# Optimization experiments

Measured on AMD Instinct MI355X. Metric: run time of the kernel, lower is better.

Reference implementation:

```python
import jax, jax.numpy as jnp
import numpy as np

EMB = 1024
HEADS = 16
HEADSIZE = EMB // HEADS
LN_EPS = 1e-5


def layernorm(x, w, b):
    # normalize over last dim (headsize)
    mu = jnp.mean(x, axis=-1, keepdims=True)
    var = jnp.var(x, axis=-1, keepdims=True)
    return (x - mu) * jax.lax.rsqrt(var + LN_EPS) * w + b


def setup_inputs() -> dict:
    key = jax.random.key(0)
    ks = jax.random.split(key, 8)
    B, S, C = 2, 2048, 2048
    x = jax.random.normal(ks[0], (B, S, EMB), dtype=jnp.float32)
    context = jax.random.normal(ks[1], (B, C, EMB), dtype=jnp.float32)
    mask = jnp.ones((B, S), dtype=jnp.float32)
    contextMask = jnp.ones((B, C), dtype=jnp.float32)
    s = 0.02
    Wq = jax.random.normal(ks[2], (EMB, EMB), dtype=jnp.float32) * s
    Wk = jax.random.normal(ks[3], (EMB, EMB), dtype=jnp.float32) * s
    Wv = jax.random.normal(ks[4], (EMB, EMB), dtype=jnp.float32) * s
    Wu = jax.random.normal(ks[5], (EMB, EMB), dtype=jnp.float32) * s
    bu = jnp.zeros((EMB,), dtype=jnp.float32)
    qln_w = jnp.ones((HEADSIZE,), dtype=jnp.float32)
    qln_b = jnp.zeros((HEADSIZE,), dtype=jnp.float32)
    kln_w = jnp.ones((HEADSIZE,), dtype=jnp.float32)
    kln_b = jnp.zeros((HEADSIZE,), dtype=jnp.float32)
    return {"x": x, "context": context, "mask": mask, "contextMask": contextMask,
            "Wq": Wq, "Wk": Wk, "Wv": Wv, "Wu": Wu, "bu": bu,
            "qln_w": qln_w, "qln_b": qln_b, "kln_w": kln_w, "kln_b": kln_b}


def reference(x, context, mask, contextMask, Wq, Wk, Wv, Wu, bu, qln_w, qln_b, kln_w, kln_b):
    B, S, E = x.shape
    C = context.shape[1]
    T = S + C
    xc = jnp.concatenate([x, context], axis=1)            # [B, T, E]
    q = (x @ Wq).reshape(B, S, HEADS, HEADSIZE)
    k = (xc @ Wk).reshape(B, T, HEADS, HEADSIZE)
    v = (xc @ Wv).reshape(B, T, HEADS, HEADSIZE)
    q = layernorm(q, qln_w, qln_b)
    k = layernorm(k, kln_w, kln_b)
    scale = E ** 0.25
    q = q / scale
    k = k / scale
    # [B, H, S, T] score matrix (explicitly materialized, as in the original)
    dot = jnp.einsum('bshd,bthd->bhst', q, k)
    mcat = jnp.concatenate([mask, contextMask], axis=1)   # [B, T]
    dotMask = mask[:, None, :, None] * mcat[:, None, None, :]  # [B,1,S,T]
    # hand-rolled masked softmax: softmax(dot*mask) * mask, renormalize
    p = jax.nn.softmax(dot * dotMask, axis=-1) * dotMask
    p = p / (jnp.sum(p, axis=-1, keepdims=True) + 1e-13)
    out = jnp.einsum('bhst,bthd->bshd', p, v).reshape(B, S, E)
    return out @ Wu + bu
```

## Files before the change

### kernel.cpp

```cpp
#include <hip/hip_runtime.h>
#include <hip/hip_bf16.h>
#include <cstdint>

#define B_SZ   2
#define S_LEN  2048
#define C_LEN  2048
#define T_LEN  4096
#define EMB_   1024
#define HEADS_ 16
#define D_     64

typedef __attribute__((ext_vector_type(8))) short bf16x8;
typedef __attribute__((ext_vector_type(4))) float f32x4;
typedef __attribute__((ext_vector_type(16))) float f32x16;
typedef __attribute__((ext_vector_type(2))) float f32x2;

__device__ __forceinline__ unsigned short f2bf(float f) {
    unsigned u = __builtin_bit_cast(unsigned, f);
    u += 0x7fffu + ((u >> 16) & 1u);
    return (unsigned short)(u >> 16);
}
__device__ __forceinline__ float bf2f(unsigned short h) {
    return __builtin_bit_cast(float, (unsigned)h << 16);
}

__global__ void build_xcb_k(const float* __restrict__ x, const float* __restrict__ ctx,
                            unsigned short* __restrict__ xcb) {
    int i = blockIdx.x * blockDim.x + threadIdx.x;
    size_t e8 = (size_t)i * 8;
    int b = (int)(e8 / ((size_t)T_LEN * EMB_));
    size_t rem = e8 % ((size_t)T_LEN * EMB_);
    int t = (int)(rem / EMB_);
    int c = (int)(rem % EMB_);
    const float* src = (t < S_LEN)
        ? &x[((size_t)b * S_LEN + t) * EMB_ + c]
        : &ctx[((size_t)b * C_LEN + (t - S_LEN)) * EMB_ + c];
    float4 v0 = ((const float4*)src)[0];
    float4 v1 = ((const float4*)src)[1];
    uint4 o;
    o.x = (unsigned)f2bf(v0.x) | ((unsigned)f2bf(v0.y) << 16);
    o.y = (unsigned)f2bf(v0.z) | ((unsigned)f2bf(v0.w) << 16);
    o.z = (unsigned)f2bf(v1.x) | ((unsigned)f2bf(v1.y) << 16);
    o.w = (unsigned)f2bf(v1.z) | ((unsigned)f2bf(v1.w) << 16);
    *(uint4*)&xcb[e8] = o;
}

__global__ void mcat_k(const float* __restrict__ mask, const float* __restrict__ cmask,
                       float* __restrict__ Mcat) {
    int i = blockIdx.x * 256 + threadIdx.x;
    int b = i / T_LEN, t = i % T_LEN;
    Mcat[i] = (t < S_LEN) ? mask[(size_t)b * S_LEN + t]
                          : cmask[(size_t)b * C_LEN + (t - S_LEN)];
}

__global__ void wtrans4_k(const float* __restrict__ W0, const float* __restrict__ W1,
                          const float* __restrict__ W2, const float* __restrict__ W3,
                          unsigned short* __restrict__ T0, unsigned short* __restrict__ T1,
                          unsigned short* __restrict__ T2, unsigned short* __restrict__ T3) {
    __shared__ __align__(16) unsigned short tile[64][72];
    int bx = blockIdx.x, by = blockIdx.y, bz = blockIdx.z;
    const float* W = (bz == 0) ? W0 : (bz == 1) ? W1 : (bz == 2) ? W2 : W3;
    unsigned short* WT = (bz == 0) ? T0 : (bz == 1) ? T1 : (bz == 2) ? T2 : T3;
    int tid = threadIdx.x;
#pragma unroll
    for (int r = 0; r < 4; ++r) {
        int idx = tid + r * 256;
        int row = idx >> 4, c4 = idx & 15;
        float4 v = ((const float4*)&W[((size_t)(by * 64 + row)) * EMB_ + bx * 64])[c4];
        tile[row][c4 * 4 + 0] = f2bf(v.x);
        tile[row][c4 * 4 + 1] = f2bf(v.y);
        tile[row][c4 * 4 + 2] = f2bf(v.z);
        tile[row][c4 * 4 + 3] = f2bf(v.w);
    }
    __syncthreads();
#pragma unroll
    for (int r = 0; r < 2; ++r) {
        int idx = tid + r * 256;
        int n = idx >> 3, k8 = idx & 7;
        uint4 o;
        unsigned q[4];
#pragma unroll
        for (int j = 0; j < 4; ++j)
            q[j] = (unsigned)tile[k8 * 8 + 2 * j][n] | ((unsigned)tile[k8 * 8 + 2 * j + 1][n] << 16);
        o.x = q[0]; o.y = q[1]; o.z = q[2]; o.w = q[3];
        *(uint4*)&WT[((size_t)(bx * 64 + n)) * EMB_ + by * 64 + k8 * 8] = o;
    }
}

__global__ __launch_bounds__(256) void gemm_qkv_fused_k(
    const unsigned short* __restrict__ A,
    const unsigned short* __restrict__ Bt,
    unsigned short* __restrict__ KF,
    unsigned short* __restrict__ VF,
    unsigned short* __restrict__ Qb,
    const float* __restrict__ qlnw, const float* __restrict__ qlnb,
    const float* __restrict__ klnw, const float* __restrict__ klnb,
    const float* __restrict__ Mcat,
    float kscale, float qscale) {
    constexpr int KTOT = 1024;
    int nt = blockIdx.x, mt = blockIdx.y;
    if (nt >= 16 && (mt & 31) >= 16) return;
    __shared__ __align__(16) unsigned short As[128 * 32];
    __shared__ __align__(16) unsigned short Bs[128 * 32];
    int in_row0 = mt * 128;
    int mode = (nt < 8) ? 0 : (nt < 16) ? 1 : 2;
    int col0 = (mode == 0) ? nt * 128 : (mode == 1) ? (nt - 8) * 128 : (nt - 16) * 128;
    int tid = threadIdx.x, w = tid >> 6, l = tid & 63, l15 = l & 15, lg = l >> 4;
    int wr = (w >> 1) * 64, wc = (w & 1) * 64;

    f32x4 zero4 = {0.f, 0.f, 0.f, 0.f};
    f32x4 acc[4][4];
#pragma unroll
    for (int i = 0; i < 4; ++i)
#pragma unroll
        for (int j = 0; j < 4; ++j) acc[i][j] = zero4;

    for (int k0 = 0; k0 < KTOT; k0 += 32) {
#pragma unroll
        for (int j = 0; j < 2; ++j) {
            int o = tid * 16 + j * 4096;
            int row = o >> 6;
            int ke = (o & 63) >> 1;
            __builtin_amdgcn_global_load_lds(
                (const __attribute__((address_space(1))) void*)&A[(size_t)(in_row0 + row) * KTOT + k0 + ke],
                (__attribute__((address_space(3))) void*)&As[o >> 1], 16, 0, 0);
            __builtin_amdgcn_global_load_lds(
                (const __attribute__((address_space(1))) void*)&Bt[(size_t)(nt * 128 + row) * KTOT + k0 + ke],
                (__attribute__((address_space(3))) void*)&Bs[o >> 1], 16, 0, 0);
        }
        __syncthreads();
        bf16x8 af[4], bf[4];
#pragma unroll
        for (int fr = 0; fr < 4; ++fr)
            af[fr] = *(const bf16x8*)&As[(wr + fr * 16 + l15) * 32 + lg * 8];
#pragma unroll
        for (int fc = 0; fc < 4; ++fc)
            bf[fc] = *(const bf16x8*)&Bs[(wc + fc * 16 + l15) * 32 + lg * 8];
#pragma unroll
        for (int fr = 0; fr < 4; ++fr)
#pragma unroll
            for (int fc = 0; fc < 4; ++fc)
                acc[fr][fc] = __builtin_amdgcn_mfma_f32_16x16x32_bf16(af[fr], bf[fc], acc[fr][fc], 0, 0, 0);
        __syncthreads();
    }

    int h = (col0 + wc) >> 6;
    float lwv[4], lbv[4];
    if (mode == 0) {
#pragma unroll
        for (int fc = 0; fc < 4; ++fc) { lwv[fc] = klnw[fc * 16 + l15]; lbv[fc] = klnb[fc * 16 + l15]; }
    } else if (mode == 2) {
#pragma unroll
        for (int fc = 0; fc < 4; ++fc) { lwv[fc] = qlnw[fc * 16 + l15]; lbv[fc] = qlnb[fc * 16 + l15]; }
    }
#pragma unroll
    for (int fr = 0; fr < 4; ++fr) {
#pragma unroll
        for (int i = 0; i < 4; ++i) {
            float mu = 0.f, rstd = 0.f;
            if (mode != 1) {
                float s  = acc[fr][0][i] + acc[fr][1][i] + acc[fr][2][i] + acc[fr][3][i];
                float s2 = acc[fr][0][i] * acc[fr][0][i] + acc[fr][1][i] * acc[fr][1][i]
                         + acc[fr][2][i] * acc[fr][2][i] + acc[fr][3][i] * acc[fr][3][i];
#pragma unroll
                for (int m = 1; m <= 8; m <<= 1) {
                    s  += __shfl_xor(s, m);
                    s2 += __shfl_xor(s2, m);
                }
                mu = s * (1.f / 64.f);
                float var = s2 * (1.f / 64.f) - mu * mu;
                rstd = rsqrtf(var + 1e-5f);
            }
            if (mode == 2) {
                int r = (mt & 31) * 128 + wr + fr * 16 + lg * 4 + i;
                int bq = mt >> 5;
                float mq = Mcat[(size_t)bq * T_LEN + r];
                size_t bh = (size_t)(bq * HEADS_ + h);
#pragma unroll
                for (int fc = 0; fc < 4; ++fc) {
                    int dh = fc * 16 + l15;
                    float o = (acc[fr][fc][i] - mu) * rstd * lwv[fc] + lbv[fc];
                    Qb[(bh * S_LEN + r) * 64 + dh] = f2bf(o * qscale * mq);
                }
            } else {
                int grow = in_row0 + wr + fr * 16 + lg * 4 + i;
                int bb = grow >> 12, t = grow & 4095;
                float mt_ = Mcat[(size_t)bb * T_LEN + t];
                size_t bh = (size_t)(bb * HEADS_ + h);
                int kt = t >> 5, t31 = t & 31;
                if (mode == 0) {
#pragma unroll
                    for (int fc = 0; fc < 4; ++fc) {
                        int dh = fc * 16 + l15;
                        float o = (acc[fr][fc][i] - mu) * rstd * lwv[fc] + lbv[fc];
                        size_t flat = (((bh * 128 + kt) * 4 + (dh >> 4)) * 64
                                       + ((dh >> 3) & 1) * 32 + t31) * 8 + (dh & 7);
                        KF[flat] = f2bf(o * kscale * mt_);
                    }
                } else {
                    int f1 = (t31 >> 4) & 1;
                    int j = ((t31 >> 3) & 1) * 4 + (t31 & 3);
                    int lofs = ((t31 >> 2) & 1) * 32;
#pragma unroll
                    for (int fc = 0; fc < 4; ++fc) {
                        int dh = fc * 16 + l15;
                        int f = (dh >> 5) * 2 + f1;
                        int ll = lofs + (dh & 31);
                        size_t flat = (((bh * 128 + kt) * 4 + f) * 64 + ll) * 8 + j;
                        VF[flat] = f2bf(acc[fr][fc][i] * mt_);
                    }
                }
            }
        }
    }
}

template <bool F32OUT>
__global__ __launch_bounds__(256) void gemm_bt_k(
    const unsigned short* __restrict__ A,
    const unsigned short* __restrict__ Bt,
    void* __restrict__ Cout,
    const float* __restrict__ bias,
    int mtiles_per_chunk, int chunk_stride) {
    constexpr int KTOT = 1024, NTOT = 1024;
    __shared__ __align__(16) unsigned short As[128 * 32];
    __shared__ __align__(16) unsigned short Bs[128 * 32];
    int nt = blockIdx.x, mt = blockIdx.y;
    int in_row0 = (mt / mtiles_per_chunk) * chunk_stride + (mt % mtiles_per_chunk) * 128;
    int out_row0 = mt * 128;
    int tid = threadIdx.x, w = tid >> 6, l = tid & 63, l15 = l & 15, lg = l >> 4;
    int wr = (w >> 1) * 64, wc = (w & 1) * 64;

    f32x4 zero4 = {0.f, 0.f, 0.f, 0.f};
    f32x4 acc[4][4];
#pragma unroll
    for (int i = 0; i < 4; ++i)
#pragma unroll
        for (int j = 0; j < 4; ++j) acc[i][j] = zero4;

    for (int k0 = 0; k0 < KTOT; k0 += 32) {
#pragma unroll
        for (int j = 0; j < 2; ++j) {
            int o = tid * 16 + j * 4096;
            int row = o >> 6;
            int ke = (o & 63) >> 1;
            __builtin_amdgcn_global_load_lds(
                (const __attribute__((address_space(1))) void*)&A[(size_t)(in_row0 + row) * KTOT + k0 + ke],
                (__attribute__((address_space(3))) void*)&As[o >> 1], 16, 0, 0);
            __builtin_amdgcn_global_load_lds(
                (const __attribute__((address_space(1))) void*)&Bt[(size_t)(nt * 128 + row) * KTOT + k0 + ke],
                (__attribute__((address_space(3))) void*)&Bs[o >> 1], 16, 0, 0);
        }
        __syncthreads();
        bf16x8 af[4], bf[4];
#pragma unroll
        for (int fr = 0; fr < 4; ++fr)
            af[fr] = *(const bf16x8*)&As[(wr + fr * 16 + l15) * 32 + lg * 8];
#pragma unroll
        for (int fc = 0; fc < 4; ++fc)
            bf[fc] = *(const bf16x8*)&Bs[(wc + fc * 16 + l15) * 32 + lg * 8];
#pragma unroll
        for (int fr = 0; fr < 4; ++fr)
#pragma unroll
            for (int fc = 0; fc < 4; ++fc)
                acc[fr][fc] = __builtin_amdgcn_mfma_f32_16x16x32_bf16(af[fr], bf[fc], acc[fr][fc], 0, 0, 0);
        __syncthreads();
    }
#pragma unroll
    for (int fr = 0; fr < 4; ++fr) {
#pragma unroll
        for (int fc = 0; fc < 4; ++fc) {
            int row = out_row0 + wr + fr * 16 + lg * 4;
            int col = nt * 128 + wc + fc * 16 + l15;
#pragma unroll
            for (int i = 0; i < 4; ++i) {
                float v = acc[fr][fc][i];
                if (F32OUT) {
                    ((float*)Cout)[(size_t)(row + i) * NTOT + col] = v + bias[col];
                } else {
                    ((unsigned short*)Cout)[(size_t)(row + i) * NTOT + col] = f2bf(v);
                }
            }
        }
    }
}

#define SOFTMAX(SA, MT, LS, PB0, PB1) do {                                        \
    f32x2 e2[8];                                                                  \
    _Pragma("unroll") for (int i_ = 0; i_ < 8; ++i_) {                            \
        e2[i_][0] = __builtin_amdgcn_exp2f(SA[2 * i_]);                           \
        e2[i_][1] = __builtin_amdgcn_exp2f(SA[2 * i_ + 1]);                       \
    }                                                                             \
    {                                                                             \
        float rsA_ = 0.f, rsB_ = 0.f;                                             \
        _Pragma("unroll") for (int i_ = 0; i_ < 8; ++i_) {                        \
            rsA_ = fmaf(e2[i_][0], MT[2 * i_], rsA_);                             \
            rsB_ = fmaf(e2[i_][1], MT[2 * i_ + 1], rsB_);                         \
        }                                                                         \
        float rs_ = rsA_ + rsB_;                                                  \
        rs_ += __shfl_xor(rs_, 32);                                               \
        (LS) += rs_;                                                              \
    }                                                                             \
    unsigned pk_[8];                                                              \
    _Pragma("unroll") for (int d_ = 0; d_ < 8; ++d_)                              \
        asm("v_cvt_pk_bf16_f32 %0, %1, %2" : "=v"(pk_[d_])                        \
            : "v"(e2[d_][0]), "v"(e2[d_][1]));                                    \
    { uint4 u0_; u0_.x=pk_[0]; u0_.y=pk_[1]; u0_.z=pk_[2]; u0_.w=pk_[3];          \
      uint4 u1_; u1_.x=pk_[4]; u1_.y=pk_[5]; u1_.z=pk_[6]; u1_.w=pk_[7];          \
      (PB0) = __builtin_bit_cast(bf16x8, u0_);                                    \
      (PB1) = __builtin_bit_cast(bf16x8, u1_); }                                  \
} while (0)

__global__ __launch_bounds__(256) void attn32_k(
    const unsigned short* __restrict__ Q,
    const unsigned short* __restrict__ KF,
    const unsigned short* __restrict__ VF,
    const float* __restrict__ Mcat,
    unsigned short* __restrict__ O) {
    __shared__ __align__(16) unsigned short Ks[4][2048];
    __shared__ __align__(16) unsigned short Vs[4][2048];
    __shared__ float OldsF[4][64][32];
    __shared__ float Llds[4][32];

    int bid = blockIdx.x;
    int xcd = bid & 7, slot = bid >> 3;
    int bh = xcd * 4 + (slot >> 4);
    int qblk = slot & 15;
    int b = bh >> 4, h = bh & 15;
    int tid = threadIdx.x;
    int w = tid >> 6;
    int lane = tid & 63;
    int l31 = lane & 31;
    int hi = lane >> 5;
    int q0 = qblk * 128;
    int qw = q0 + w * 32;

    const unsigned short* KFb_ = KF + (size_t)bh * 262144;
    const unsigned short* VFb_ = VF + (size_t)bh * 262144;
    const float* Mb = Mcat + (size_t)b * T_LEN;

    bf16x8 qf[4];
    {
        const unsigned short* Qp = Q + ((size_t)bh * S_LEN + qw + l31) * 64 + hi * 8;
#pragma unroll
        for (int s = 0; s < 4; ++s) qf[s] = *(const bf16x8*)(Qp + s * 16);
    }

    f32x16 Z16;
#pragma unroll
    for (int i = 0; i < 16; ++i) Z16[i] = 0.f;
    f32x16 acc0 = Z16, acc1 = Z16;
    float lS = 0.f;

#define STAGE(BUF, KT) do {                                                        \
    __builtin_amdgcn_global_load_lds(                                              \
        (const __attribute__((address_space(1))) void*)(KFb_ + (size_t)(KT) * 2048 + tid * 8), \
        (__attribute__((address_space(3))) void*)&Ks[BUF][tid * 8], 16, 0, 0);     \
    __builtin_amdgcn_global_load_lds(                                              \
        (const __attribute__((address_space(1))) void*)(VFb_ + (size_t)(KT) * 2048 + tid * 8), \
        (__attribute__((address_space(3))) void*)&Vs[BUF][tid * 8], 16, 0, 0);     \
} while (0)

    STAGE(0, 0); STAGE(1, 1);
    __syncthreads();

    for (int it = 0; it < 64; ++it) {
        int base = (it & 1) << 1;
        int kt0 = it * 2;
        if (it < 63) {
            STAGE(base ^ 2, kt0 + 2);
            STAGE((base ^ 2) + 1, kt0 + 3);
        }
        const float* mb0 = Mb + kt0 * 32 + 4 * hi;
        float4 am0 = *(const float4*)(mb0);
        float4 am1 = *(const float4*)(mb0 + 8);
        float4 am2 = *(const float4*)(mb0 + 16);
        float4 am3 = *(const float4*)(mb0 + 24);
        float4 bm0 = *(const float4*)(mb0 + 32);
        float4 bm1 = *(const float4*)(mb0 + 40);
        float4 bm2 = *(const float4*)(mb0 + 48);
        float4 bm3 = *(const float4*)(mb0 + 56);
        bf16x8 kfrA[4], vfrA[4], kfrB[4], vfrB[4];
#pragma unroll
        for (int s = 0; s < 4; ++s) {
            kfrA[s] = *(const bf16x8*)&Ks[base][s * 512 + lane * 8];
            vfrA[s] = *(const bf16x8*)&Vs[base][s * 512 + lane * 8];
            kfrB[s] = *(const bf16x8*)&Ks[base + 1][s * 512 + lane * 8];
            vfrB[s] = *(const bf16x8*)&Vs[base + 1][s * 512 + lane * 8];
        }
        f32x16 saA = Z16, saB = Z16;
#pragma unroll
        for (int s = 0; s < 4; ++s) {
            saA = __builtin_amdgcn_mfma_f32_32x32x16_bf16(kfrA[s], qf[s], saA, 0, 0, 0);
            saB = __builtin_amdgcn_mfma_f32_32x32x16_bf16(kfrB[s], qf[s], saB, 0, 0, 0);
        }
        float mtA_[16], mtB_[16];
        mtA_[0] = am0.x; mtA_[1] = am0.y; mtA_[2]  = am0.z; mtA_[3]  = am0.w;
        mtA_[4] = am1.x; mtA_[5] = am1.y; mtA_[6]  = am1.z; mtA_[7]  = am1.w;
        mtA_[8] = am2.x; mtA_[9] = am2.y; mtA_[10] = am2.z; mtA_[11] = am2.w;
        mtA_[12] = am3.x; mtA_[13] = am3.y; mtA_[14] = am3.z; mtA_[15] = am3.w;
        mtB_[0] = bm0.x; mtB_[1] = bm0.y; mtB_[2]  = bm0.z; mtB_[3]  = bm0.w;
        mtB_[4] = bm1.x; mtB_[5] = bm1.y; mtB_[6]  = bm1.z; mtB_[7]  = bm1.w;
        mtB_[8] = bm2.x; mtB_[9] = bm2.y; mtB_[10] = bm2.z; mtB_[11] = bm2.w;
        mtB_[12] = bm3.x; mtB_[13] = bm3.y; mtB_[14] = bm3.z; mtB_[15] = bm3.w;
        bf16x8 p0A, p1A, p0B, p1B;
        SOFTMAX(saA, mtA_, lS, p0A, p1A);
        SOFTMAX(saB, mtB_, lS, p0B, p1B);
        acc0 = __builtin_amdgcn_mfma_f32_32x32x16_bf16(vfrA[0], p0A, acc0, 0, 0, 0);
        acc1 = __builtin_amdgcn_mfma_f32_32x32x16_bf16(vfrA[2], p0A, acc1, 0, 0, 0);
        acc0 = __builtin_amdgcn_mfma_f32_32x32x16_bf16(vfrA[1], p1A, acc0, 0, 0, 0);
        acc1 = __builtin_amdgcn_mfma_f32_32x32x16_bf16(vfrA[3], p1A, acc1, 0, 0, 0);
        acc0 = __builtin_amdgcn_mfma_f32_32x32x16_bf16(vfrB[0], p0B, acc0, 0, 0, 0);
        acc1 = __builtin_amdgcn_mfma_f32_32x32x16_bf16(vfrB[2], p0B, acc1, 0, 0, 0);
        acc0 = __builtin_amdgcn_mfma_f32_32x32x16_bf16(vfrB[1], p1B, acc0, 0, 0, 0);
        acc1 = __builtin_amdgcn_mfma_f32_32x32x16_bf16(vfrB[3], p1B, acc1, 0, 0, 0);
        __syncthreads();
    }
#undef STAGE

#pragma unroll
    for (int r = 0; r < 16; ++r) {
        int dl = (r & 3) + 8 * (r >> 2) + 4 * hi;
        OldsF[w][dl][l31] = acc0[r];
        OldsF[w][dl + 32][l31] = acc1[r];
    }
    if (hi == 0) Llds[w][l31] = lS;
    __syncthreads();
    {
        int rr = lane >> 1, hf = lane & 1;
        float L = Llds[w][rr];
        float invL = 1.f / (L + 1e-13f);
        float mqz = Mb[q0 + w * 32 + rr];
        invL = (mqz != 0.f) ? invL : 0.f;
        float v_[32];
#pragma unroll
        for (int dd = 0; dd < 32; ++dd)
            v_[dd] = OldsF[w][hf * 32 + dd][rr] * invL;
        unsigned po_[16];
#pragma unroll
        for (int d2 = 0; d2 < 16; ++d2)
            asm("v_cvt_pk_bf16_f32 %0, %1, %2" : "=v"(po_[d2]) : "v"(v_[2*d2]), "v"(v_[2*d2+1]));
        unsigned short* Orow = &O[((size_t)b * S_LEN + qw + rr) * EMB_ + h * 64 + hf * 32];
#pragma unroll
        for (int i = 0; i < 4; ++i) {
            uint4 st;
            st.x = po_[4*i]; st.y = po_[4*i+1]; st.z = po_[4*i+2]; st.w = po_[4*i+3];
            *(uint4*)(Orow + i * 8) = st;
        }
    }
}

extern "C" void kernel_launch(void* const* d_in, const int* in_sizes, int n_in,
                              void* d_out, int out_size, void* d_ws, size_t ws_size,
                              hipStream_t stream) {
    const float* x     = (const float*)d_in[0];
    const float* ctx   = (const float*)d_in[1];
    const float* mask  = (const float*)d_in[2];
    const float* cmask = (const float*)d_in[3];
    const float* Wq    = (const float*)d_in[4];
    const float* Wk    = (const float*)d_in[5];
    const float* Wv    = (const float*)d_in[6];
    const float* Wu    = (const float*)d_in[7];
    const float* bu    = (const float*)d_in[8];
    const float* qlnw  = (const float*)d_in[9];
    const float* qlnb  = (const float*)d_in[10];
    const float* klnw  = (const float*)d_in[11];
    const float* klnb  = (const float*)d_in[12];

    unsigned short* ws = (unsigned short*)d_ws;
    unsigned short* xcb = ws + 0;
    unsigned short* WkT = ws + 8388608;
    unsigned short* WvT = ws + 9437184;
    unsigned short* WqT = ws + 10485760;
    unsigned short* WuT = ws + 12582912;
    unsigned short* Qb  = ws + 13631488;
    unsigned short* KFb = ws + 17825792;
    unsigned short* VFb = ws + 26214400;
    unsigned short* Ob  = ws + 0;
    float* Mcat         = (float*)(ws + 34603008);

    const float scale = 0.17677669529663687f;
    const float qscale = 0.17677669529663687f * 1.4426950408889634f;

    build_xcb_k<<<4096, 256, 0, stream>>>(x, ctx, xcb);
    mcat_k<<<32, 256, 0, stream>>>(mask, cmask, Mcat);
    wtrans4_k<<<dim3(16, 16, 4), 256, 0, stream>>>(Wk, Wv, Wq, Wu, WkT, WvT, WqT, WuT);

    gemm_qkv_fused_k<<<dim3(24, 64), 256, 0, stream>>>(
        xcb, WkT, KFb, VFb, Qb, qlnw, qlnb, klnw, klnb, Mcat, scale, qscale);

    attn32_k<<<512, 256, 0, stream>>>(Qb, KFb, VFb, Mcat, Ob);

    gemm_bt_k<true><<<dim3(8, 32), 256, 0, stream>>>(Ob, WuT, d_out, bu, 32, 4096);
}
```

Baseline: 230.5 us.

## Merge prep kernels, shrink output GEMM tiles, load V directly to registers

Folds the three preprocessing kernels (bf16 conversion of x/context, mask concat, weight transposes) into one launch, removing two launch gaps. The output projection GEMM now uses 64-row M tiles, so the grid doubles to 512 blocks to fill more CUs. The attention kernel stops staging V through LDS and reads each lane's V fragment straight from global memory into registers, which cuts LDS traffic and footprint but relies on global/L2 latency being hidden inside the loop.

```diff
diff --git a/kernel.cpp b/kernel.cpp
--- a/kernel.cpp
+++ b/kernel.cpp
@@ -24,66 +24,68 @@
     return __builtin_bit_cast(float, (unsigned)h << 16);
 }
 
-__global__ void build_xcb_k(const float* __restrict__ x, const float* __restrict__ ctx,
-                            unsigned short* __restrict__ xcb) {
-    int i = blockIdx.x * blockDim.x + threadIdx.x;
-    size_t e8 = (size_t)i * 8;
-    int b = (int)(e8 / ((size_t)T_LEN * EMB_));
-    size_t rem = e8 % ((size_t)T_LEN * EMB_);
-    int t = (int)(rem / EMB_);
-    int c = (int)(rem % EMB_);
-    const float* src = (t < S_LEN)
-        ? &x[((size_t)b * S_LEN + t) * EMB_ + c]
-        : &ctx[((size_t)b * C_LEN + (t - S_LEN)) * EMB_ + c];
-    float4 v0 = ((const float4*)src)[0];
-    float4 v1 = ((const float4*)src)[1];
-    uint4 o;
-    o.x = (unsigned)f2bf(v0.x) | ((unsigned)f2bf(v0.y) << 16);
-    o.y = (unsigned)f2bf(v0.z) | ((unsigned)f2bf(v0.w) << 16);
-    o.z = (unsigned)f2bf(v1.x) | ((unsigned)f2bf(v1.y) << 16);
-    o.w = (unsigned)f2bf(v1.z) | ((unsigned)f2bf(v1.w) << 16);
-    *(uint4*)&xcb[e8] = o;
-}
-
-__global__ void mcat_k(const float* __restrict__ mask, const float* __restrict__ cmask,
-                       float* __restrict__ Mcat) {
-    int i = blockIdx.x * 256 + threadIdx.x;
-    int b = i / T_LEN, t = i % T_LEN;
-    Mcat[i] = (t < S_LEN) ? mask[(size_t)b * S_LEN + t]
-                          : cmask[(size_t)b * C_LEN + (t - S_LEN)];
-}
-
-__global__ void wtrans4_k(const float* __restrict__ W0, const float* __restrict__ W1,
-                          const float* __restrict__ W2, const float* __restrict__ W3,
-                          unsigned short* __restrict__ T0, unsigned short* __restrict__ T1,
-                          unsigned short* __restrict__ T2, unsigned short* __restrict__ T3) {
+__global__ void prep_k(const float* __restrict__ x, const float* __restrict__ ctx,
+                       unsigned short* __restrict__ xcb,
+                       const float* __restrict__ mask, const float* __restrict__ cmask,
+                       float* __restrict__ Mcat,
+                       const float* __restrict__ W0, const float* __restrict__ W1,
+                       const float* __restrict__ W2, const float* __restrict__ W3,
+                       unsigned short* __restrict__ T0, unsigned short* __restrict__ T1,
+                       unsigned short* __restrict__ T2, unsigned short* __restrict__ T3) {
     __shared__ __align__(16) unsigned short tile[64][72];
-    int bx = blockIdx.x, by = blockIdx.y, bz = blockIdx.z;
-    const float* W = (bz == 0) ? W0 : (bz == 1) ? W1 : (bz == 2) ? W2 : W3;
-    unsigned short* WT = (bz == 0) ? T0 : (bz == 1) ? T1 : (bz == 2) ? T2 : T3;
+    int bid = blockIdx.x;
     int tid = threadIdx.x;
-#pragma unroll
-    for (int r = 0; r < 4; ++r) {
-        int idx = tid + r * 256;
-        int row = idx >> 4, c4 = idx & 15;
-        float4 v = ((const float4*)&W[((size_t)(by * 64 + row)) * EMB_ + bx * 64])[c4];
-        tile[row][c4 * 4 + 0] = f2bf(v.x);
-        tile[row][c4 * 4 + 1] = f2bf(v.y);
-        tile[row][c4 * 4 + 2] = f2bf(v.z);
-        tile[row][c4 * 4 + 3] = f2bf(v.w);
-    }
-    __syncthreads();
-#pragma unroll
-    for (int r = 0; r < 2; ++r) {
-        int idx = tid + r * 256;
-        int n = idx >> 3, k8 = idx & 7;
+    if (bid < 4096) {
+        int i = bid * 256 + tid;
+        size_t e8 = (size_t)i * 8;
+        int b = (int)(e8 / ((size_t)T_LEN * EMB_));
+        size_t rem = e8 % ((size_t)T_LEN * EMB_);
+        int t = (int)(rem / EMB_);
+        int c = (int)(rem % EMB_);
+        const float* src = (t < S_LEN)
+            ? &x[((size_t)b * S_LEN + t) * EMB_ + c]
+            : &ctx[((size_t)b * C_LEN + (t - S_LEN)) * EMB_ + c];
+        float4 v0 = ((const float4*)src)[0];
+        float4 v1 = ((const float4*)src)[1];
         uint4 o;
-        unsigned q[4];
-#pragma unroll
-        for (int j = 0; j < 4; ++j)
-            q[j] = (unsigned)tile[k8 * 8 + 2 * j][n] | ((unsigned)tile[k8 * 8 + 2 * j + 1][n] << 16);
-        o.x = q[0]; o.y = q[1]; o.z = q[2]; o.w = q[3];
-        *(uint4*)&WT[((size_t)(bx * 64 + n)) * EMB_ + by * 64 + k8 * 8] = o;
+        o.x = (unsigned)f2bf(v0.x) | ((unsigned)f2bf(v0.y) << 16);
+        o.y = (unsigned)f2bf(v0.z) | ((unsigned)f2bf(v0.w) << 16);
+        o.z = (unsigned)f2bf(v1.x) | ((unsigned)f2bf(v1.y) << 16);
+        o.w = (unsigned)f2bf(v1.z) | ((unsigned)f2bf(v1.w) << 16);
+        *(uint4*)&xcb[e8] = o;
+    } else if (bid < 5120) {
+        int idx = bid - 4096;
+        int bz = idx >> 8, rm = idx & 255, by = rm >> 4, bx = rm & 15;
+        const float* W = (bz == 0) ? W0 : (bz == 1) ? W1 : (bz == 2) ? W2 : W3;
+        unsigned short* WT = (bz == 0) ? T0 : (bz == 1) ? T1 : (bz == 2) ? T2 : T3;
+#pragma unroll
+        for (int r = 0; r < 4; ++r) {
+            int id2 = tid + r * 256;
+            int row = id2 >> 4, c4 = id2 & 15;
+            float4 v = ((const float4*)&W[((size_t)(by * 64 + row)) * EMB_ + bx * 64])[c4];
+            tile[row][c4 * 4 + 0] = f2bf(v.x);
+            tile[row][c4 * 4 + 1] = f2bf(v.y);
+            tile[row][c4 * 4 + 2] = f2bf(v.z);
+            tile[row][c4 * 4 + 3] = f2bf(v.w);
+        }
+        __syncthreads();
+#pragma unroll
+        for (int r = 0; r < 2; ++r) {
+            int id2 = tid + r * 256;
+            int n = id2 >> 3, k8 = id2 & 7;
+            uint4 o;
+            unsigned q[4];
+#pragma unroll
+            for (int j = 0; j < 4; ++j)
+                q[j] = (unsigned)tile[k8 * 8 + 2 * j][n] | ((unsigned)tile[k8 * 8 + 2 * j + 1][n] << 16);
+            o.x = q[0]; o.y = q[1]; o.z = q[2]; o.w = q[3];
+            *(uint4*)&WT[((size_t)(bx * 64 + n)) * EMB_ + by * 64 + k8 * 8] = o;
+        }
+    } else {
+        int i = (bid - 5120) * 256 + tid;
+        int b = i / T_LEN, t = i % T_LEN;
+        Mcat[i] = (t < S_LEN) ? mask[(size_t)b * S_LEN + t]
+                              : cmask[(size_t)b * C_LEN + (t - S_LEN)];
     }
 }
 
@@ -215,72 +217,68 @@
     }
 }
 
-template <bool F32OUT>
-__global__ __launch_bounds__(256) void gemm_bt_k(
+__global__ __launch_bounds__(256) void gemm_bt64_k(
     const unsigned short* __restrict__ A,
     const unsigned short* __restrict__ Bt,
-    void* __restrict__ Cout,
-    const float* __restrict__ bias,
-    int mtiles_per_chunk, int chunk_stride) {
+    float* __restrict__ Cout,
+    const float* __restrict__ bias) {
     constexpr int KTOT = 1024, NTOT = 1024;
-    __shared__ __align__(16) unsigned short As[128 * 32];
+    __shared__ __align__(16) unsigned short As[64 * 32];
     __shared__ __align__(16) unsigned short Bs[128 * 32];
     int nt = blockIdx.x, mt = blockIdx.y;
-    int in_row0 = (mt / mtiles_per_chunk) * chunk_stride + (mt % mtiles_per_chunk) * 128;
-    int out_row0 = mt * 128;
+    int row0 = mt * 64;
     int tid = threadIdx.x, w = tid >> 6, l = tid & 63, l15 = l & 15, lg = l >> 4;
-    int wr = (w >> 1) * 64, wc = (w & 1) * 64;
+    int wr = (w >> 1) * 32, wc = (w & 1) * 64;
 
     f32x4 zero4 = {0.f, 0.f, 0.f, 0.f};
-    f32x4 acc[4][4];
-#pragma unroll
-    for (int i = 0; i < 4; ++i)
+    f32x4 acc[2][4];
+#pragma unroll
+    for (int i = 0; i < 2; ++i)
 #pragma unroll
         for (int j = 0; j < 4; ++j) acc[i][j] = zero4;
 
     for (int k0 = 0; k0 < KTOT; k0 += 32) {
+        {
+            int o = tid * 16;
+            int row = o >> 6;
+            int ke = (o & 63) >> 1;
+            __builtin_amdgcn_global_load_lds(
+                (const __attribute__((address_space(1))) void*)&A[(size_t)(row0 + row) * KTOT + k0 + ke],
+                (__attribute__((address_space(3))) void*)&As[o >> 1], 16, 0, 0);
+        }
 #pragma unroll
         for (int j = 0; j < 2; ++j) {
             int o = tid * 16 + j * 4096;
             int row = o >> 6;
             int ke = (o & 63) >> 1;
             __builtin_amdgcn_global_load_lds(
-                (const __attribute__((address_space(1))) void*)&A[(size_t)(in_row0 + row) * KTOT + k0 + ke],
-                (__attribute__((address_space(3))) void*)&As[o >> 1], 16, 0, 0);
-            __builtin_amdgcn_global_load_lds(
                 (const __attribute__((address_space(1))) void*)&Bt[(size_t)(nt * 128 + row) * KTOT + k0 + ke],
                 (__attribute__((address_space(3))) void*)&Bs[o >> 1], 16, 0, 0);
         }
         __syncthreads();
-        bf16x8 af[4], bf[4];
-#pragma unroll
-        for (int fr = 0; fr < 4; ++fr)
+        bf16x8 af[2], bf[4];
+#pragma unroll
+        for (int fr = 0; fr < 2; ++fr)
             af[fr] = *(const bf16x8*)&As[(wr + fr * 16 + l15) * 32 + lg * 8];
 #pragma unroll
         for (int fc = 0; fc < 4; ++fc)
             bf[fc] = *(const bf16x8*)&Bs[(wc + fc * 16 + l15) * 32 + lg * 8];
 #pragma unroll
-        for (int fr = 0; fr < 4; ++fr)
+        for (int fr = 0; fr < 2; ++fr)
 #pragma unroll
             for (int fc = 0; fc < 4; ++fc)
                 acc[fr][fc] = __builtin_amdgcn_mfma_f32_16x16x32_bf16(af[fr], bf[fc], acc[fr][fc], 0, 0, 0);
         __syncthreads();
     }
 #pragma unroll
-    for (int fr = 0; fr < 4; ++fr) {
+    for (int fr = 0; fr < 2; ++fr) {
 #pragma unroll
         for (int fc = 0; fc < 4; ++fc) {
-            int row = out_row0 + wr + fr * 16 + lg * 4;
+            int row = row0 + wr + fr * 16 + lg * 4;
             int col = nt * 128 + wc + fc * 16 + l15;
 #pragma unroll
-            for (int i = 0; i < 4; ++i) {
-                float v = acc[fr][fc][i];
-                if (F32OUT) {
-                    ((float*)Cout)[(size_t)(row + i) * NTOT + col] = v + bias[col];
-                } else {
-                    ((unsigned short*)Cout)[(size_t)(row + i) * NTOT + col] = f2bf(v);
-                }
-            }
+            for (int i = 0; i < 4; ++i)
+                Cout[(size_t)(row + i) * NTOT + col] = acc[fr][fc][i] + bias[col];
         }
     }
 }
@@ -318,7 +316,6 @@
     const float* __restrict__ Mcat,
     unsigned short* __restrict__ O) {
     __shared__ __align__(16) unsigned short Ks[4][2048];
-    __shared__ __align__(16) unsigned short Vs[4][2048];
     __shared__ float OldsF[4][64][32];
     __shared__ float Llds[4][32];
 
@@ -336,7 +333,7 @@
     int qw = q0 + w * 32;
 
     const unsigned short* KFb_ = KF + (size_t)bh * 262144;
-    const unsigned short* VFb_ = VF + (size_t)bh * 262144;
+    const unsigned short* VFl = VF + (size_t)bh * 262144 + lane * 8;
     const float* Mb = Mcat + (size_t)b * T_LEN;
 
     bf16x8 qf[4];
@@ -352,25 +349,31 @@
     f32x16 acc0 = Z16, acc1 = Z16;
     float lS = 0.f;
 
-#define STAGE(BUF, KT) do {                                                        \
+#define STAGEK(BUF, KT) do {                                                       \
     __builtin_amdgcn_global_load_lds(                                              \
         (const __attribute__((address_space(1))) void*)(KFb_ + (size_t)(KT) * 2048 + tid * 8), \
         (__attribute__((address_space(3))) void*)&Ks[BUF][tid * 8], 16, 0, 0);     \
-    __builtin_amdgcn_global_load_lds(                                              \
-        (const __attribute__((address_space(1))) void*)(VFb_ + (size_t)(KT) * 2048 + tid * 8), \
-        (__attribute__((address_space(3))) void*)&Vs[BUF][tid * 8], 16, 0, 0);     \
 } while (0)
 
-    STAGE(0, 0); STAGE(1, 1);
+    STAGEK(0, 0); STAGEK(1, 1);
     __syncthreads();
 
     for (int it = 0; it < 64; ++it) {
         int base = (it & 1) << 1;
         int kt0 = it * 2;
         if (it < 63) {
-            STAGE(base ^ 2, kt0 + 2);
-            STAGE((base ^ 2) + 1, kt0 + 3);
-        }
+            STAGEK(base ^ 2, kt0 + 2);
+            STAGEK((base ^ 2) + 1, kt0 + 3);
+        }
+        const unsigned short* pv = VFl + (size_t)kt0 * 2048;
+        uint4 vA0 = *(const uint4*)(pv);
+        uint4 vA1 = *(const uint4*)(pv + 512);
+        uint4 vA2 = *(const uint4*)(pv + 1024);
+        uint4 vA3 = *(const uint4*)(pv + 1536);
+        uint4 vB0 = *(const uint4*)(pv + 2048);
+        uint4 vB1 = *(const uint4*)(pv + 2560);
+        uint4 vB2 = *(const uint4*)(pv + 3072);
+        uint4 vB3 = *(const uint4*)(pv + 3584);
         const float* mb0 = Mb + kt0 * 32 + 4 * hi;
         float4 am0 = *(const float4*)(mb0);
         float4 am1 = *(const float4*)(mb0 + 8);
@@ -380,13 +383,11 @@
         float4 bm1 = *(const float4*)(mb0 + 40);
         float4 bm2 = *(const float4*)(mb0 + 48);
         float4 bm3 = *(const float4*)(mb0 + 56);
-        bf16x8 kfrA[4], vfrA[4], kfrB[4], vfrB[4];
+        bf16x8 kfrA[4], kfrB[4];
 #pragma unroll
         for (int s = 0; s < 4; ++s) {
             kfrA[s] = *(const bf16x8*)&Ks[base][s * 512 + lane * 8];
-            vfrA[s] = *(const bf16x8*)&Vs[base][s * 512 + lane * 8];
             kfrB[s] = *(const bf16x8*)&Ks[base + 1][s * 512 + lane * 8];
-            vfrB[s] = *(const bf16x8*)&Vs[base + 1][s * 512 + lane * 8];
         }
         f32x16 saA = Z16, saB = Z16;
 #pragma unroll
@@ -406,17 +407,17 @@
         bf16x8 p0A, p1A, p0B, p1B;
         SOFTMAX(saA, mtA_, lS, p0A, p1A);
         SOFTMAX(saB, mtB_, lS, p0B, p1B);
-        acc0 = __builtin_amdgcn_mfma_f32_32x32x16_bf16(vfrA[0], p0A, acc0, 0, 0, 0);
-        acc1 = __builtin_amdgcn_mfma_f32_32x32x16_bf16(vfrA[2], p0A, acc1, 0, 0, 0);
-        acc0 = __builtin_amdgcn_mfma_f32_32x32x16_bf16(vfrA[1], p1A, acc0, 0, 0, 0);
-        acc1 = __builtin_amdgcn_mfma_f32_32x32x16_bf16(vfrA[3], p1A, acc1, 0, 0, 0);
-        acc0 = __builtin_amdgcn_mfma_f32_32x32x16_bf16(vfrB[0], p0B, acc0, 0, 0, 0);
-        acc1 = __builtin_amdgcn_mfma_f32_32x32x16_bf16(vfrB[2], p0B, acc1, 0, 0, 0);
-        acc0 = __builtin_amdgcn_mfma_f32_32x32x16_bf16(vfrB[1], p1B, acc0, 0, 0, 0);
-        acc1 = __builtin_amdgcn_mfma_f32_32x32x16_bf16(vfrB[3], p1B, acc1, 0, 0, 0);
-        __syncthreads();
-    }
-#undef STAGE
+        acc0 = __builtin_amdgcn_mfma_f32_32x32x16_bf16(__builtin_bit_cast(bf16x8, vA0), p0A, acc0, 0, 0, 0);
+        acc1 = __builtin_amdgcn_mfma_f32_32x32x16_bf16(__builtin_bit_cast(bf16x8, vA2), p0A, acc1, 0, 0, 0);
+        acc0 = __builtin_amdgcn_mfma_f32_32x32x16_bf16(__builtin_bit_cast(bf16x8, vA1), p1A, acc0, 0, 0, 0);
+        acc1 = __builtin_amdgcn_mfma_f32_32x32x16_bf16(__builtin_bit_cast(bf16x8, vA3), p1A, acc1, 0, 0, 0);
+        acc0 = __builtin_amdgcn_mfma_f32_32x32x16_bf16(__builtin_bit_cast(bf16x8, vB0), p0B, acc0, 0, 0, 0);
+        acc1 = __builtin_amdgcn_mfma_f32_32x32x16_bf16(__builtin_bit_cast(bf16x8, vB2), p0B, acc1, 0, 0, 0);
+        acc0 = __builtin_amdgcn_mfma_f32_32x32x16_bf16(__builtin_bit_cast(bf16x8, vB1), p1B, acc0, 0, 0, 0);
+        acc1 = __builtin_amdgcn_mfma_f32_32x32x16_bf16(__builtin_bit_cast(bf16x8, vB3), p1B, acc1, 0, 0, 0);
+        __syncthreads();
+    }
+#undef STAGEK
 
 #pragma unroll
     for (int r = 0; r < 16; ++r) {
@@ -482,14 +483,13 @@
     const float scale = 0.17677669529663687f;
     const float qscale = 0.17677669529663687f * 1.4426950408889634f;
 
-    build_xcb_k<<<4096, 256, 0, stream>>>(x, ctx, xcb);
-    mcat_k<<<32, 256, 0, stream>>>(mask, cmask, Mcat);
-    wtrans4_k<<<dim3(16, 16, 4), 256, 0, stream>>>(Wk, Wv, Wq, Wu, WkT, WvT, WqT, WuT);
+    prep_k<<<5152, 256, 0, stream>>>(x, ctx, xcb, mask, cmask, Mcat,
+                                     Wk, Wv, Wq, Wu, WkT, WvT, WqT, WuT);
 
     gemm_qkv_fused_k<<<dim3(24, 64), 256, 0, stream>>>(
         xcb, WkT, KFb, VFb, Qb, qlnw, qlnb, klnw, klnb, Mcat, scale, qscale);
 
     attn32_k<<<512, 256, 0, stream>>>(Qb, KFb, VFb, Mcat, Ob);
 
-    gemm_bt_k<true><<<dim3(8, 32), 256, 0, stream>>>(Ob, WuT, d_out, bu, 32, 4096);
-}
+    gemm_bt64_k<<<dim3(8, 64), 256, 0, stream>>>(Ob, WuT, (float*)d_out, bu);
+}
```

Measured after the change: 227.8 us. Within noise of the previous version (-1.2%).
